# Kernel tuning notes

Hardware: AMD Instinct MI355X
Metric: run time of the kernel (lower is better)

The kernel has to match this reference:

```python
import jax, jax.numpy as jnp
import numpy as np

NUM_HEADS = 8


def setup_inputs() -> dict:
    key = jax.random.key(0)
    ks = jax.random.split(key, 14)
    B, S, E = 4, 2048, 512
    D_EMO = 64
    s = 1.0 / np.sqrt(E)
    inp = {
        "query": jax.random.normal(ks[0], (B, S, E), jnp.float32),
        "key": jax.random.normal(ks[1], (B, S, E), jnp.float32),
        "value": jax.random.normal(ks[2], (B, S, E), jnp.float32),
        "emotional_context": jax.random.normal(ks[3], (B, D_EMO), jnp.float32),
        "Wq": jax.random.normal(ks[4], (E, E), jnp.float32) * s,
        "bq": jnp.zeros((E,), jnp.float32),
        "Wk": jax.random.normal(ks[5], (E, E), jnp.float32) * s,
        "bk": jnp.zeros((E,), jnp.float32),
        "Wv": jax.random.normal(ks[6], (E, E), jnp.float32) * s,
        "bv": jnp.zeros((E,), jnp.float32),
        "Wo": jax.random.normal(ks[7], (E, E), jnp.float32) * s,
        "bo": jnp.zeros((E,), jnp.float32),
        "emo_bias": jax.random.normal(ks[8], (NUM_HEADS, 1, 1), jnp.float32),
    }
    return inp


def reference(query, key, value, emotional_context, Wq, bq, Wk, bk, Wv, bv, Wo, bo, emo_bias):
    B, S, E = query.shape
    H = NUM_HEADS
    D = E // H
    scale = 1.0 / np.sqrt(D).astype(np.float32)

    def proj(x, W, b):  # [B,S,E] -> [B,H,S,D]
        return (x @ W.T + b).reshape(B, S, H, D).transpose(0, 2, 1, 3)

    Q = proj(query, Wq, bq)
    K = proj(key, Wk, bk)
    V = proj(value, Wv, bv)

    # [B,H,S,S] score tensor (the memory-bound hot spot)
    scores = jnp.einsum("bhqd,bhkd->bhqk", Q, K) * scale
    scores = scores + emo_bias[None]  # additive per-head emotional bias
    # multiplicative emotional modulation: sigmoid of mean context, per batch
    mod = 0.5 + 0.5 * jax.nn.sigmoid(emotional_context.mean(axis=-1))  # [B]
    scores = scores * mod[:, None, None, None]

    attn = jax.nn.softmax(scores, axis=-1)
    # dropout(0.1) is identity in eval mode
    attended = jnp.einsum("bhqk,bhkd->bhqd", attn, V)
    attended = attended.transpose(0, 2, 1, 3).reshape(B, S, E)
    output = attended @ Wo.T + bo
    return output, attn.mean(axis=1)
```

## Files before the change

### kernel.cpp

```cpp
#include <hip/hip_runtime.h>

#define BATCH 4
#define SEQ   2048
#define EMB   512
#define HEADS 8
#define HD    64

typedef _Float16 half2_t __attribute__((ext_vector_type(2)));
typedef _Float16 half4_t __attribute__((ext_vector_type(4)));
typedef _Float16 half8_t __attribute__((ext_vector_type(8)));
typedef float    f32x4   __attribute__((ext_vector_type(4)));

#if __has_builtin(__builtin_amdgcn_exp2f)
#define EXP2F(x) __builtin_amdgcn_exp2f(x)
#else
#define EXP2F(x) exp2f(x)
#endif
#define LOG2E 1.44269504088896f

#define PKRTZ(a, b) __builtin_bit_cast(half2_t, __builtin_amdgcn_cvt_pkrtz((a), (b)))

__global__ void mod_kernel(const float* __restrict__ emo, float* __restrict__ modv){
    int lane = threadIdx.x;
    for (int b = 0; b < BATCH; ++b){
        float v = emo[b*64 + lane];
        #pragma unroll
        for (int off = 32; off >= 1; off >>= 1) v += __shfl_xor(v, off, 64);
        if (lane == 0){
            float mean = v * (1.0f/64.0f);
            float sig  = 1.0f/(1.0f + __expf(-mean));
            modv[b] = 0.5f + 0.5f*sig;
        }
    }
}

__device__ inline half8_t cvt8(const float* p){
    float4 v0 = *(const float4*)p;
    float4 v1 = *(const float4*)(p + 4);
    half8_t r;
    r[0]=(_Float16)v0.x; r[1]=(_Float16)v0.y; r[2]=(_Float16)v0.z; r[3]=(_Float16)v0.w;
    r[4]=(_Float16)v1.x; r[5]=(_Float16)v1.y; r[6]=(_Float16)v1.z; r[7]=(_Float16)v1.w;
    return r;
}

__device__ inline half8_t cvt8v(float4 v0, float4 v1){
    half8_t r;
    r[0]=(_Float16)v0.x; r[1]=(_Float16)v0.y; r[2]=(_Float16)v0.z; r[3]=(_Float16)v0.w;
    r[4]=(_Float16)v1.x; r[5]=(_Float16)v1.y; r[6]=(_Float16)v1.z; r[7]=(_Float16)v1.w;
    return r;
}

__global__ __launch_bounds__(256) void qkv_kernel(
    const float* __restrict__ X0, const float* __restrict__ X1, const float* __restrict__ X2,
    const float* __restrict__ W0, const float* __restrict__ W1, const float* __restrict__ W2,
    const float* __restrict__ b0, const float* __restrict__ b1, const float* __restrict__ b2,
    _Float16* __restrict__ o0, _Float16* __restrict__ o1, _Float16* __restrict__ o2)
{
    const int z = blockIdx.z;
    const float* X    = (z==0) ? X0 : (z==1) ? X1 : X2;
    const float* W    = (z==0) ? W0 : (z==1) ? W1 : W2;
    const float* bias = (z==0) ? b0 : (z==1) ? b1 : b2;
    _Float16*  out    = (z==0) ? o0 : (z==1) ? o1 : o2;

    __shared__ _Float16 lA[2][128*64];
    __shared__ _Float16 lB[2][64*64];

    const int tid  = threadIdx.x;
    const int wid  = tid >> 6;
    const int lane = tid & 63;
    const int l16  = lane & 15;
    const int g    = lane >> 4;
    const int l7   = l16 & 7;
    const int mb = blockIdx.x;
    const int nb = blockIdx.y;
    const int wm = (wid >> 1)*64;
    const int wn = (wid & 1)*32;
    const int tR = tid >> 3;
    const int c8 = tid & 7;

    #pragma unroll
    for (int p = 0; p < 4; ++p){
        const int R = p*32 + tR;
        half8_t h = cvt8(X + (size_t)(mb*128 + R)*EMB + c8*8);
        *(half8_t*)(&lA[0][R*64 + ((c8 ^ (R & 7))*8)]) = h;
    }
    #pragma unroll
    for (int p = 0; p < 2; ++p){
        const int R = p*32 + tR;
        half8_t h = cvt8(W + (size_t)(nb*64 + R)*EMB + c8*8);
        *(half8_t*)(&lB[0][R*64 + ((c8 ^ (R & 7))*8)]) = h;
    }
    __syncthreads();

    f32x4 acc[4][2] = {};
    int cur = 0;
    for (int ks = 0; ks < 8; ++ks){
        float4 xa0[4], xa1[4], wb0[2], wb1[2];
        if (ks < 7){
            #pragma unroll
            for (int p = 0; p < 4; ++p){
                const float* px = X + (size_t)(mb*128 + p*32 + tR)*EMB + (ks+1)*64 + c8*8;
                xa0[p] = *(const float4*)px;
                xa1[p] = *(const float4*)(px + 4);
            }
            #pragma unroll
            for (int p = 0; p < 2; ++p){
                const float* pw = W + (size_t)(nb*64 + p*32 + tR)*EMB + (ks+1)*64 + c8*8;
                wb0[p] = *(const float4*)pw;
                wb1[p] = *(const float4*)(pw + 4);
            }
        }
        #pragma unroll
        for (int u = 0; u < 2; ++u){
            half8_t af[4], bf[2];
            #pragma unroll
            for (int i = 0; i < 4; ++i){
                const int rA = wm + i*16 + l16;
                af[i] = *(half8_t*)(&lA[cur][rA*64 + (((u*4 + g) ^ l7)*8)]);
            }
            #pragma unroll
            for (int j = 0; j < 2; ++j){
                const int rB = wn + j*16 + l16;
                bf[j] = *(half8_t*)(&lB[cur][rB*64 + (((u*4 + g) ^ l7)*8)]);
            }
            #pragma unroll
            for (int i = 0; i < 4; ++i)
                #pragma unroll
                for (int j = 0; j < 2; ++j)
                    acc[i][j] = __builtin_amdgcn_mfma_f32_16x16x32_f16(af[i], bf[j], acc[i][j], 0, 0, 0);
        }
        if (ks < 7){
            #pragma unroll
            for (int p = 0; p < 4; ++p){
                const int R = p*32 + tR;
                *(half8_t*)(&lA[cur^1][R*64 + ((c8 ^ (R & 7))*8)]) = cvt8v(xa0[p], xa1[p]);
            }
            #pragma unroll
            for (int p = 0; p < 2; ++p){
                const int R = p*32 + tR;
                *(half8_t*)(&lB[cur^1][R*64 + ((c8 ^ (R & 7))*8)]) = cvt8v(wb0[p], wb1[p]);
            }
        }
        __syncthreads();
        cur ^= 1;
    }
    #pragma unroll
    for (int j = 0; j < 2; ++j){
        const int nn  = nb*64 + wn + j*16 + l16;
        const float bn = bias[nn];
        const int h = nn >> 6, d = nn & 63;
        #pragma unroll
        for (int i = 0; i < 4; ++i){
            #pragma unroll
            for (int r = 0; r < 4; ++r){
                const int m  = mb*128 + wm + i*16 + 4*g + r;
                const int bb2 = m >> 11, s = m & 2047;
                const int bh  = bb2*8 + h;
                const float v = acc[i][j][r] + bn;
                size_t idx;
                if (z == 2)
                    idx = ((size_t)(bh*128 + (s>>4))*2 + (d>>5))*512
                        + (size_t)((((s>>2)&3)*16 + (d&15))*8 + ((d>>4)&1)*4 + (s&3));
                else
                    idx = ((size_t)(bh*128 + (s>>4))*2 + (d>>5))*512
                        + (size_t)((((d>>3)&3)*16 + (s&15))*8 + (d&7));
                out[idx] = (_Float16)v;
            }
        }
    }
}

__global__ __launch_bounds__(256) void pv_kernel(
    const _Float16* __restrict__ Qf, const _Float16* __restrict__ Kf,
    const _Float16* __restrict__ Vf, const float* __restrict__ emo_bias,
    const float* __restrict__ modv, _Float16* __restrict__ attended,
    float* __restrict__ Ldenom)
{
    __shared__ _Float16 lK[2][4096];
    __shared__ _Float16 lV[2][4096];

    const int tid  = threadIdx.x;
    const int lane = tid & 63;
    const int l16  = lane & 15;
    const int g    = lane >> 4;
    const int w    = tid >> 6;
    const int n    = blockIdx.x;
    const int work = (n & 7)*128 + (n >> 3);
    const int qt   = work & 31;
    const int bh   = work >> 5;
    const int b    = bh >> 3, h = bh & 7;
    const int q0   = qt*64 + w*16;

    const float mod = modv[b];
    const float sm2 = 0.125f * mod * LOG2E;
    const float bm2 = emo_bias[h] * mod * LOG2E;

    const size_t fB = (size_t)bh * 128;

    half8_t qf[2];
    #pragma unroll
    for (int c = 0; c < 2; ++c)
        qf[c] = *(const half8_t*)(Qf + ((fB + (q0>>4))*2 + c)*512 + lane*8);

    {
        const _Float16* gk = Kf + fB*1024;
        const _Float16* gv = Vf + fB*1024;
        *(half8_t*)(&lK[0][tid*8])        = *(const half8_t*)(gk + tid*8);
        *(half8_t*)(&lK[0][2048 + tid*8]) = *(const half8_t*)(gk + 2048 + tid*8);
        *(half8_t*)(&lV[0][tid*8])        = *(const half8_t*)(gv + tid*8);
        *(half8_t*)(&lV[0][2048 + tid*8]) = *(const half8_t*)(gv + 2048 + tid*8);
    }
    __syncthreads();

    f32x4 acc[4] = {};
    float lsum = 0.f;
    int cur = 0;
    for (int grp = 0; grp < SEQ/64; ++grp){
        half8_t rk0, rk1, rv0, rv1;
        if (grp < SEQ/64 - 1){
            const _Float16* gk = Kf + (fB + (size_t)(grp+1)*4)*1024;
            const _Float16* gv = Vf + (fB + (size_t)(grp+1)*4)*1024;
            rk0 = *(const half8_t*)(gk + tid*8);
            rk1 = *(const half8_t*)(gk + 2048 + tid*8);
            rv0 = *(const half8_t*)(gv + tid*8);
            rv1 = *(const half8_t*)(gv + 2048 + tid*8);
        }
        const _Float16* kb = &lK[cur][0];
        const _Float16* vb = &lV[cur][0];
        #pragma unroll
        for (int t = 0; t < 4; ++t){
            half8_t k0 = *(const half8_t*)(kb + (t*2+0)*512 + lane*8);
            half8_t k1 = *(const half8_t*)(kb + (t*2+1)*512 + lane*8);
            f32x4 s = {};
            s = __builtin_amdgcn_mfma_f32_16x16x32_f16(k0, qf[0], s, 0, 0, 0);
            s = __builtin_amdgcn_mfma_f32_16x16x32_f16(k1, qf[1], s, 0, 0, 0);
            float e0 = EXP2F(s[0]*sm2 + bm2);
            float e1 = EXP2F(s[1]*sm2 + bm2);
            float e2 = EXP2F(s[2]*sm2 + bm2);
            float e3 = EXP2F(s[3]*sm2 + bm2);
            lsum += (e0 + e1) + (e2 + e3);
            half2_t plo = PKRTZ(e0, e1), phi = PKRTZ(e2, e3);
            half4_t pf  = __builtin_shufflevector(plo, phi, 0, 1, 2, 3);
            half8_t vp0 = *(const half8_t*)(vb + (t*2+0)*512 + lane*8);
            half8_t vp1 = *(const half8_t*)(vb + (t*2+1)*512 + lane*8);
            half4_t v0 = __builtin_shufflevector(vp0, vp0, 0, 1, 2, 3);
            half4_t v1 = __builtin_shufflevector(vp0, vp0, 4, 5, 6, 7);
            half4_t v2 = __builtin_shufflevector(vp1, vp1, 0, 1, 2, 3);
            half4_t v3 = __builtin_shufflevector(vp1, vp1, 4, 5, 6, 7);
            acc[0] = __builtin_amdgcn_mfma_f32_16x16x16f16(pf, v0, acc[0], 0, 0, 0);
            acc[1] = __builtin_amdgcn_mfma_f32_16x16x16f16(pf, v1, acc[1], 0, 0, 0);
            acc[2] = __builtin_amdgcn_mfma_f32_16x16x16f16(pf, v2, acc[2], 0, 0, 0);
            acc[3] = __builtin_amdgcn_mfma_f32_16x16x16f16(pf, v3, acc[3], 0, 0, 0);
        }
        if (grp < SEQ/64 - 1){
            *(half8_t*)(&lK[cur^1][tid*8])        = rk0;
            *(half8_t*)(&lK[cur^1][2048 + tid*8]) = rk1;
            *(half8_t*)(&lV[cur^1][tid*8])        = rv0;
            *(half8_t*)(&lV[cur^1][2048 + tid*8]) = rv1;
        }
        __syncthreads();
        cur ^= 1;
    }

    lsum += __shfl_xor(lsum, 16, 64);
    lsum += __shfl_xor(lsum, 32, 64);
    if (g == 0) Ldenom[(size_t)bh*SEQ + q0 + l16] = lsum;
    const float inv = 1.0f / lsum;
    float invr[4];
    #pragma unroll
    for (int r = 0; r < 4; ++r)
        invr[r] = __shfl(inv, 4*g + r, 64);
    #pragma unroll
    for (int c = 0; c < 4; ++c)
        #pragma unroll
        for (int r = 0; r < 4; ++r)
            attended[(size_t)(b*SEQ + q0 + 4*g + r)*EMB + h*64 + 16*c + l16]
                = (_Float16)(acc[c][r] * invr[r]);
}

__global__ __launch_bounds__(256) void mean_kernel(
    const _Float16* __restrict__ Qf, const _Float16* __restrict__ Kf,
    const float* __restrict__ emo_bias, const float* __restrict__ modv,
    const float* __restrict__ Ldenom, float* __restrict__ mean_out)
{
    const int tid  = threadIdx.x;
    const int w    = tid >> 6;
    const int lane = tid & 63;
    const int l16  = lane & 15;
    const int g    = lane >> 4;
    const int n    = blockIdx.x;
    const int work = (n & 7)*512 + (n >> 3);
    const int b    = work >> 10;
    const int ky   = (work >> 7) & 7;
    const int qt   = work & 127;
    const int q0   = qt * 16;
    const int k0w  = ky*256 + w*64;

    const float mod = modv[b];
    const float sm2 = 0.125f * mod * LOG2E;

    f32x4 msum[4] = {};
    for (int hp = 0; hp < HEADS/2; ++hp){
        const int h0 = 2*hp, h1 = 2*hp + 1;
        const size_t lo0 = (size_t)(b*HEADS + h0) * SEQ;
        const size_t lo1 = (size_t)(b*HEADS + h1) * SEQ;
        const size_t f0  = (size_t)(b*HEADS + h0) * 128;
        const size_t f1  = (size_t)(b*HEADS + h1) * 128;
        const float bm20 = emo_bias[h0] * mod * LOG2E;
        const float bm21 = emo_bias[h1] * mod * LOG2E;
        half8_t qa0 = *(const half8_t*)(Qf + ((f0 + (q0>>4))*2 + 0)*512 + lane*8);
        half8_t qa1 = *(const half8_t*)(Qf + ((f0 + (q0>>4))*2 + 1)*512 + lane*8);
        half8_t qb0 = *(const half8_t*)(Qf + ((f1 + (q0>>4))*2 + 0)*512 + lane*8);
        half8_t qb1 = *(const half8_t*)(Qf + ((f1 + (q0>>4))*2 + 1)*512 + lane*8);
        float iA[4], iB[4];
        #pragma unroll
        for (int r = 0; r < 4; ++r){
            iA[r] = 1.0f / Ldenom[lo0 + q0 + 4*g + r];
            iB[r] = 1.0f / Ldenom[lo1 + q0 + 4*g + r];
        }
        #pragma unroll
        for (int j = 0; j < 4; ++j){
            const int kc = (k0w >> 4) + j;
            half8_t ka0 = *(const half8_t*)(Kf + ((f0 + kc)*2 + 0)*512 + lane*8);
            half8_t ka1 = *(const half8_t*)(Kf + ((f0 + kc)*2 + 1)*512 + lane*8);
            half8_t kb0 = *(const half8_t*)(Kf + ((f1 + kc)*2 + 0)*512 + lane*8);
            half8_t kb1 = *(const half8_t*)(Kf + ((f1 + kc)*2 + 1)*512 + lane*8);
            f32x4 sA = {}, sB = {};
            sA = __builtin_amdgcn_mfma_f32_16x16x32_f16(qa0, ka0, sA, 0, 0, 0);
            sA = __builtin_amdgcn_mfma_f32_16x16x32_f16(qa1, ka1, sA, 0, 0, 0);
            sB = __builtin_amdgcn_mfma_f32_16x16x32_f16(qb0, kb0, sB, 0, 0, 0);
            sB = __builtin_amdgcn_mfma_f32_16x16x32_f16(qb1, kb1, sB, 0, 0, 0);
            #pragma unroll
            for (int r = 0; r < 4; ++r){
                float pa = EXP2F(sA[r]*sm2 + bm20) * iA[r];
                float pb = EXP2F(sB[r]*sm2 + bm21) * iB[r];
                msum[j][r] += pa + pb;
            }
        }
    }
    #pragma unroll
    for (int j = 0; j < 4; ++j)
        #pragma unroll
        for (int r = 0; r < 4; ++r)
            mean_out[(size_t)(b*SEQ + q0 + 4*g + r)*SEQ + k0w + j*16 + l16]
                = msum[j][r] * (1.0f/HEADS);
}

__global__ __launch_bounds__(256) void outproj_kernel(
    const _Float16* __restrict__ A, const float* __restrict__ W,
    const float* __restrict__ bias, float* __restrict__ out)
{
    __shared__ _Float16 lA[2][128*64];
    __shared__ _Float16 lB[2][64*64];

    const int tid  = threadIdx.x;
    const int wid  = tid >> 6;
    const int lane = tid & 63;
    const int l16  = lane & 15;
    const int g    = lane >> 4;
    const int l7   = l16 & 7;
    const int mb = blockIdx.x;
    const int nb = blockIdx.y;
    const int wm = (wid >> 1)*64;
    const int wn = (wid & 1)*32;
    const int tR = tid >> 3;
    const int c8 = tid & 7;

    #pragma unroll
    for (int p = 0; p < 4; ++p){
        const int R = p*32 + tR;
        half8_t h = *(const half8_t*)(A + (size_t)(mb*128 + R)*EMB + c8*8);
        *(half8_t*)(&lA[0][R*64 + ((c8 ^ (R & 7))*8)]) = h;
    }
    #pragma unroll
    for (int p = 0; p < 2; ++p){
        const int R = p*32 + tR;
        half8_t h = cvt8(W + (size_t)(nb*64 + R)*EMB + c8*8);
        *(half8_t*)(&lB[0][R*64 + ((c8 ^ (R & 7))*8)]) = h;
    }
    __syncthreads();

    f32x4 acc[4][2] = {};
    int cur = 0;
    for (int ks = 0; ks < 8; ++ks){
        half8_t ra[4];
        float4 wb0[2], wb1[2];
        if (ks < 7){
            #pragma unroll
            for (int p = 0; p < 4; ++p)
                ra[p] = *(const half8_t*)(A + (size_t)(mb*128 + p*32 + tR)*EMB + (ks+1)*64 + c8*8);
            #pragma unroll
            for (int p = 0; p < 2; ++p){
                const float* pw = W + (size_t)(nb*64 + p*32 + tR)*EMB + (ks+1)*64 + c8*8;
                wb0[p] = *(const float4*)pw;
                wb1[p] = *(const float4*)(pw + 4);
            }
        }
        #pragma unroll
        for (int u = 0; u < 2; ++u){
            half8_t af[4], bf[2];
            #pragma unroll
            for (int i = 0; i < 4; ++i){
                const int rA = wm + i*16 + l16;
                af[i] = *(half8_t*)(&lA[cur][rA*64 + (((u*4 + g) ^ l7)*8)]);
            }
            #pragma unroll
            for (int j = 0; j < 2; ++j){
                const int rB = wn + j*16 + l16;
                bf[j] = *(half8_t*)(&lB[cur][rB*64 + (((u*4 + g) ^ l7)*8)]);
            }
            #pragma unroll
            for (int i = 0; i < 4; ++i)
                #pragma unroll
                for (int j = 0; j < 2; ++j)
                    acc[i][j] = __builtin_amdgcn_mfma_f32_16x16x32_f16(af[i], bf[j], acc[i][j], 0, 0, 0);
        }
        if (ks < 7){
            #pragma unroll
            for (int p = 0; p < 4; ++p){
                const int R = p*32 + tR;
                *(half8_t*)(&lA[cur^1][R*64 + ((c8 ^ (R & 7))*8)]) = ra[p];
            }
            #pragma unroll
            for (int p = 0; p < 2; ++p){
                const int R = p*32 + tR;
                *(half8_t*)(&lB[cur^1][R*64 + ((c8 ^ (R & 7))*8)]) = cvt8v(wb0[p], wb1[p]);
            }
        }
        __syncthreads();
        cur ^= 1;
    }
    #pragma unroll
    for (int j = 0; j < 2; ++j){
        const int nn = nb*64 + wn + j*16 + l16;
        const float bn = bias[nn];
        #pragma unroll
        for (int i = 0; i < 4; ++i)
            #pragma unroll
            for (int r = 0; r < 4; ++r){
                const int m = mb*128 + wm + i*16 + 4*g + r;
                out[(size_t)m*EMB + nn] = acc[i][j][r] + bn;
            }
    }
}

extern "C" void kernel_launch(void* const* d_in, const int* in_sizes, int n_in,
                              void* d_out, int out_size, void* d_ws, size_t ws_size,
                              hipStream_t stream)
{
    const float* query = (const float*)d_in[0];
    const float* key_  = (const float*)d_in[1];
    const float* value = (const float*)d_in[2];
    const float* emo   = (const float*)d_in[3];
    const float* Wq = (const float*)d_in[4];
    const float* bq = (const float*)d_in[5];
    const float* Wk = (const float*)d_in[6];
    const float* bk = (const float*)d_in[7];
    const float* Wv = (const float*)d_in[8];
    const float* bv = (const float*)d_in[9];
    const float* Wo = (const float*)d_in[10];
    const float* bo = (const float*)d_in[11];
    const float* emo_bias = (const float*)d_in[12];

    const size_t NTOK = (size_t)BATCH * SEQ * EMB;
    _Float16* ws       = (_Float16*)d_ws;
    _Float16* Qp       = ws;
    _Float16* Kp       = ws + NTOK;
    _Float16* Vt       = ws + 2*NTOK;
    _Float16* attended = ws + 3*NTOK;

    float* out0     = (float*)d_out;
    float* mean_out = out0 + NTOK;
    float* Ldenom   = out0;
    float* modv     = out0 + (size_t)BATCH*HEADS*SEQ;

    mod_kernel<<<1, 64, 0, stream>>>(emo, modv);
    qkv_kernel<<<dim3(64, 8, 3), 256, 0, stream>>>(query, key_, value, Wq, Wk, Wv,
                                                   bq, bk, bv, Qp, Kp, Vt);
    pv_kernel<<<BATCH*HEADS*(SEQ/64), 256, 0, stream>>>(Qp, Kp, Vt, emo_bias, modv, attended, Ldenom);
    mean_kernel<<<BATCH*(SEQ/16)*(SEQ/256), 256, 0, stream>>>(Qp, Kp, emo_bias, modv, Ldenom, mean_out);
    outproj_kernel<<<dim3(64, 8), 256, 0, stream>>>(attended, Wo, bo, out0);
}
```

Before: 177.3 us.

## Single-buffer GEMM LDS, add setprio around MFMA, split PV loop phases

The QKV and out-projection GEMMs drop LDS double buffering in favour of a single buffer with an extra barrier, halving shared memory per block so more blocks can fit per CU. The MFMA sections in all three kernels are wrapped in s_setprio to favour matrix issue. The attention inner loop is split into separate QK, exp and PV phases to batch the MFMAs. Float-to-half conversion now uses packed round-toward-zero instructions, which changes rounding slightly and adds a sync that may cost latency hiding.

Result: no change. 176.3 us (-0.6%).

```diff
diff --git a/kernel.cpp b/kernel.cpp
--- a/kernel.cpp
+++ b/kernel.cpp
@@ -34,20 +34,15 @@
     }
 }
 
+__device__ inline half8_t cvt8pk(float4 v0, float4 v1){
+    half2_t p0 = PKRTZ(v0.x, v0.y), p1 = PKRTZ(v0.z, v0.w);
+    half2_t p2 = PKRTZ(v1.x, v1.y), p3 = PKRTZ(v1.z, v1.w);
+    half4_t a = __builtin_shufflevector(p0, p1, 0, 1, 2, 3);
+    half4_t b = __builtin_shufflevector(p2, p3, 0, 1, 2, 3);
+    return __builtin_shufflevector(a, b, 0, 1, 2, 3, 4, 5, 6, 7);
+}
 __device__ inline half8_t cvt8(const float* p){
-    float4 v0 = *(const float4*)p;
-    float4 v1 = *(const float4*)(p + 4);
-    half8_t r;
-    r[0]=(_Float16)v0.x; r[1]=(_Float16)v0.y; r[2]=(_Float16)v0.z; r[3]=(_Float16)v0.w;
-    r[4]=(_Float16)v1.x; r[5]=(_Float16)v1.y; r[6]=(_Float16)v1.z; r[7]=(_Float16)v1.w;
-    return r;
-}
-
-__device__ inline half8_t cvt8v(float4 v0, float4 v1){
-    half8_t r;
-    r[0]=(_Float16)v0.x; r[1]=(_Float16)v0.y; r[2]=(_Float16)v0.z; r[3]=(_Float16)v0.w;
-    r[4]=(_Float16)v1.x; r[5]=(_Float16)v1.y; r[6]=(_Float16)v1.z; r[7]=(_Float16)v1.w;
-    return r;
+    return cvt8pk(*(const float4*)p, *(const float4*)(p + 4));
 }
 
 __global__ __launch_bounds__(256) void qkv_kernel(
@@ -62,8 +57,8 @@
     const float* bias = (z==0) ? b0 : (z==1) ? b1 : b2;
     _Float16*  out    = (z==0) ? o0 : (z==1) ? o1 : o2;
 
-    __shared__ _Float16 lA[2][128*64];
-    __shared__ _Float16 lB[2][64*64];
+    __shared__ _Float16 lA[128*64];
+    __shared__ _Float16 lB[64*64];
 
     const int tid  = threadIdx.x;
     const int wid  = tid >> 6;
@@ -81,19 +76,16 @@
     #pragma unroll
     for (int p = 0; p < 4; ++p){
         const int R = p*32 + tR;
-        half8_t h = cvt8(X + (size_t)(mb*128 + R)*EMB + c8*8);
-        *(half8_t*)(&lA[0][R*64 + ((c8 ^ (R & 7))*8)]) = h;
+        *(half8_t*)(lA + R*64 + ((c8 ^ (R & 7))*8)) = cvt8(X + (size_t)(mb*128 + R)*EMB + c8*8);
     }
     #pragma unroll
     for (int p = 0; p < 2; ++p){
         const int R = p*32 + tR;
-        half8_t h = cvt8(W + (size_t)(nb*64 + R)*EMB + c8*8);
-        *(half8_t*)(&lB[0][R*64 + ((c8 ^ (R & 7))*8)]) = h;
+        *(half8_t*)(lB + R*64 + ((c8 ^ (R & 7))*8)) = cvt8(W + (size_t)(nb*64 + R)*EMB + c8*8);
     }
     __syncthreads();
 
     f32x4 acc[4][2] = {};
-    int cur = 0;
     for (int ks = 0; ks < 8; ++ks){
         float4 xa0[4], xa1[4], wb0[2], wb1[2];
         if (ks < 7){
@@ -110,18 +102,19 @@
                 wb1[p] = *(const float4*)(pw + 4);
             }
         }
+        __builtin_amdgcn_s_setprio(1);
         #pragma unroll
         for (int u = 0; u < 2; ++u){
             half8_t af[4], bf[2];
             #pragma unroll
             for (int i = 0; i < 4; ++i){
                 const int rA = wm + i*16 + l16;
-                af[i] = *(half8_t*)(&lA[cur][rA*64 + (((u*4 + g) ^ l7)*8)]);
+                af[i] = *(half8_t*)(lA + rA*64 + (((u*4 + g) ^ l7)*8));
             }
             #pragma unroll
             for (int j = 0; j < 2; ++j){
                 const int rB = wn + j*16 + l16;
-                bf[j] = *(half8_t*)(&lB[cur][rB*64 + (((u*4 + g) ^ l7)*8)]);
+                bf[j] = *(half8_t*)(lB + rB*64 + (((u*4 + g) ^ l7)*8));
             }
             #pragma unroll
             for (int i = 0; i < 4; ++i)
@@ -129,20 +122,21 @@
                 for (int j = 0; j < 2; ++j)
                     acc[i][j] = __builtin_amdgcn_mfma_f32_16x16x32_f16(af[i], bf[j], acc[i][j], 0, 0, 0);
         }
+        __builtin_amdgcn_s_setprio(0);
+        __syncthreads();
         if (ks < 7){
             #pragma unroll
             for (int p = 0; p < 4; ++p){
                 const int R = p*32 + tR;
-                *(half8_t*)(&lA[cur^1][R*64 + ((c8 ^ (R & 7))*8)]) = cvt8v(xa0[p], xa1[p]);
+                *(half8_t*)(lA + R*64 + ((c8 ^ (R & 7))*8)) = cvt8pk(xa0[p], xa1[p]);
             }
             #pragma unroll
             for (int p = 0; p < 2; ++p){
                 const int R = p*32 + tR;
-                *(half8_t*)(&lB[cur^1][R*64 + ((c8 ^ (R & 7))*8)]) = cvt8v(wb0[p], wb1[p]);
-            }
-        }
-        __syncthreads();
-        cur ^= 1;
+                *(half8_t*)(lB + R*64 + ((c8 ^ (R & 7))*8)) = cvt8pk(wb0[p], wb1[p]);
+            }
+            __syncthreads();
+        }
     }
     #pragma unroll
     for (int j = 0; j < 2; ++j){
@@ -183,13 +177,12 @@
     const int lane = tid & 63;
     const int l16  = lane & 15;
     const int g    = lane >> 4;
-    const int w    = tid >> 6;
     const int n    = blockIdx.x;
     const int work = (n & 7)*128 + (n >> 3);
     const int qt   = work & 31;
     const int bh   = work >> 5;
     const int b    = bh >> 3, h = bh & 7;
-    const int q0   = qt*64 + w*16;
+    const int q0   = qt*64 + (tid >> 6)*16;
 
     const float mod = modv[b];
     const float sm2 = 0.125f * mod * LOG2E;
@@ -227,31 +220,44 @@
         }
         const _Float16* kb = &lK[cur][0];
         const _Float16* vb = &lV[cur][0];
+        f32x4 s[4];
+        __builtin_amdgcn_s_setprio(1);
         #pragma unroll
         for (int t = 0; t < 4; ++t){
             half8_t k0 = *(const half8_t*)(kb + (t*2+0)*512 + lane*8);
             half8_t k1 = *(const half8_t*)(kb + (t*2+1)*512 + lane*8);
-            f32x4 s = {};
-            s = __builtin_amdgcn_mfma_f32_16x16x32_f16(k0, qf[0], s, 0, 0, 0);
-            s = __builtin_amdgcn_mfma_f32_16x16x32_f16(k1, qf[1], s, 0, 0, 0);
-            float e0 = EXP2F(s[0]*sm2 + bm2);
-            float e1 = EXP2F(s[1]*sm2 + bm2);
-            float e2 = EXP2F(s[2]*sm2 + bm2);
-            float e3 = EXP2F(s[3]*sm2 + bm2);
+            f32x4 zz = {};
+            zz = __builtin_amdgcn_mfma_f32_16x16x32_f16(k0, qf[0], zz, 0, 0, 0);
+            zz = __builtin_amdgcn_mfma_f32_16x16x32_f16(k1, qf[1], zz, 0, 0, 0);
+            s[t] = zz;
+        }
+        __builtin_amdgcn_s_setprio(0);
+        half4_t pf[4];
+        #pragma unroll
+        for (int t = 0; t < 4; ++t){
+            float e0 = EXP2F(s[t][0]*sm2 + bm2);
+            float e1 = EXP2F(s[t][1]*sm2 + bm2);
+            float e2 = EXP2F(s[t][2]*sm2 + bm2);
+            float e3 = EXP2F(s[t][3]*sm2 + bm2);
             lsum += (e0 + e1) + (e2 + e3);
             half2_t plo = PKRTZ(e0, e1), phi = PKRTZ(e2, e3);
-            half4_t pf  = __builtin_shufflevector(plo, phi, 0, 1, 2, 3);
+            pf[t] = __builtin_shufflevector(plo, phi, 0, 1, 2, 3);
+        }
+        __builtin_amdgcn_s_setprio(1);
+        #pragma unroll
+        for (int t = 0; t < 4; ++t){
             half8_t vp0 = *(const half8_t*)(vb + (t*2+0)*512 + lane*8);
             half8_t vp1 = *(const half8_t*)(vb + (t*2+1)*512 + lane*8);
             half4_t v0 = __builtin_shufflevector(vp0, vp0, 0, 1, 2, 3);
             half4_t v1 = __builtin_shufflevector(vp0, vp0, 4, 5, 6, 7);
             half4_t v2 = __builtin_shufflevector(vp1, vp1, 0, 1, 2, 3);
             half4_t v3 = __builtin_shufflevector(vp1, vp1, 4, 5, 6, 7);
-            acc[0] = __builtin_amdgcn_mfma_f32_16x16x16f16(pf, v0, acc[0], 0, 0, 0);
-            acc[1] = __builtin_amdgcn_mfma_f32_16x16x16f16(pf, v1, acc[1], 0, 0, 0);
-            acc[2] = __builtin_amdgcn_mfma_f32_16x16x16f16(pf, v2, acc[2], 0, 0, 0);
-            acc[3] = __builtin_amdgcn_mfma_f32_16x16x16f16(pf, v3, acc[3], 0, 0, 0);
-        }
+            acc[0] = __builtin_amdgcn_mfma_f32_16x16x16f16(pf[t], v0, acc[0], 0, 0, 0);
+            acc[1] = __builtin_amdgcn_mfma_f32_16x16x16f16(pf[t], v1, acc[1], 0, 0, 0);
+            acc[2] = __builtin_amdgcn_mfma_f32_16x16x16f16(pf[t], v2, acc[2], 0, 0, 0);
+            acc[3] = __builtin_amdgcn_mfma_f32_16x16x16f16(pf[t], v3, acc[3], 0, 0, 0);
+        }
+        __builtin_amdgcn_s_setprio(0);
         if (grp < SEQ/64 - 1){
             *(half8_t*)(&lK[cur^1][tid*8])        = rk0;
             *(half8_t*)(&lK[cur^1][2048 + tid*8]) = rk1;
@@ -350,8 +356,8 @@
     const _Float16* __restrict__ A, const float* __restrict__ W,
     const float* __restrict__ bias, float* __restrict__ out)
 {
-    __shared__ _Float16 lA[2][128*64];
-    __shared__ _Float16 lB[2][64*64];
+    __shared__ _Float16 lA[128*64];
+    __shared__ _Float16 lB[64*64];
 
     const int tid  = threadIdx.x;
     const int wid  = tid >> 6;
@@ -369,19 +375,17 @@
     #pragma unroll
     for (int p = 0; p < 4; ++p){
         const int R = p*32 + tR;
-        half8_t h = *(const half8_t*)(A + (size_t)(mb*128 + R)*EMB + c8*8);
-        *(half8_t*)(&lA[0][R*64 + ((c8 ^ (R & 7))*8)]) = h;
+        *(half8_t*)(lA + R*64 + ((c8 ^ (R & 7))*8)) =
+            *(const half8_t*)(A + (size_t)(mb*128 + R)*EMB + c8*8);
     }
     #pragma unroll
     for (int p = 0; p < 2; ++p){
         const int R = p*32 + tR;
-        half8_t h = cvt8(W + (size_t)(nb*64 + R)*EMB + c8*8);
-        *(half8_t*)(&lB[0][R*64 + ((c8 ^ (R & 7))*8)]) = h;
+        *(half8_t*)(lB + R*64 + ((c8 ^ (R & 7))*8)) = cvt8(W + (size_t)(nb*64 + R)*EMB + c8*8);
     }
     __syncthreads();
 
     f32x4 acc[4][2] = {};
-    int cur = 0;
     for (int ks = 0; ks < 8; ++ks){
         half8_t ra[4];
         float4 wb0[2], wb1[2];
@@ -396,18 +400,19 @@
                 wb1[p] = *(const float4*)(pw + 4);
             }
         }
+        __builtin_amdgcn_s_setprio(1);
         #pragma unroll
         for (int u = 0; u < 2; ++u){
             half8_t af[4], bf[2];
             #pragma unroll
             for (int i = 0; i < 4; ++i){
                 const int rA = wm + i*16 + l16;
-                af[i] = *(half8_t*)(&lA[cur][rA*64 + (((u*4 + g) ^ l7)*8)]);
+                af[i] = *(half8_t*)(lA + rA*64 + (((u*4 + g) ^ l7)*8));
             }
             #pragma unroll
             for (int j = 0; j < 2; ++j){
                 const int rB = wn + j*16 + l16;
-                bf[j] = *(half8_t*)(&lB[cur][rB*64 + (((u*4 + g) ^ l7)*8)]);
+                bf[j] = *(half8_t*)(lB + rB*64 + (((u*4 + g) ^ l7)*8));
             }
             #pragma unroll
             for (int i = 0; i < 4; ++i)
@@ -415,20 +420,21 @@
                 for (int j = 0; j < 2; ++j)
                     acc[i][j] = __builtin_amdgcn_mfma_f32_16x16x32_f16(af[i], bf[j], acc[i][j], 0, 0, 0);
         }
+        __builtin_amdgcn_s_setprio(0);
+        __syncthreads();
         if (ks < 7){
             #pragma unroll
             for (int p = 0; p < 4; ++p){
                 const int R = p*32 + tR;
-                *(half8_t*)(&lA[cur^1][R*64 + ((c8 ^ (R & 7))*8)]) = ra[p];
+                *(half8_t*)(lA + R*64 + ((c8 ^ (R & 7))*8)) = ra[p];
             }
             #pragma unroll
             for (int p = 0; p < 2; ++p){
                 const int R = p*32 + tR;
-                *(half8_t*)(&lB[cur^1][R*64 + ((c8 ^ (R & 7))*8)]) = cvt8v(wb0[p], wb1[p]);
-            }
-        }
-        __syncthreads();
-        cur ^= 1;
+                *(half8_t*)(lB + R*64 + ((c8 ^ (R & 7))*8)) = cvt8pk(wb0[p], wb1[p]);
+            }
+            __syncthreads();
+        }
     }
     #pragma unroll
     for (int j = 0; j < 2; ++j){
```
